# Kernel optimization log

Hardware: AMD Instinct MI355X
Metric: run time of the kernel (lower is better)

The kernel has to match this reference:

```python
import jax, jax.numpy as jnp
import numpy as np

SIZE = 128
N_ATOMS = 100000
N_BONDS = 400000
N_PAIRS = 400000
N_ANGLES = 800000
LN_EPS = 1e-5


def _layernorm(h, w, b):
    m = jnp.mean(h, axis=-1, keepdims=True)
    v = jnp.mean(jnp.square(h - m), axis=-1, keepdims=True)
    return (h - m) * jax.lax.rsqrt(v + LN_EPS) * w + b


def _forward(x, bond_x, sc_pair_x, angles,
             W_bm, W_sc, W1, b1, W2, b2,
             ln1_w, ln1_b, ln2_w, ln2_b,
             bond_idx, sc_idx, angles_idx):
    n_atoms = x.shape[0]
    n_bonds = bond_x.shape[0]

    # ---- sublayer 1: bond message passing ----
    h = _layernorm(x, ln1_w, ln1_b)                       # [n_atoms, d]
    # aggregate angle features onto bonds
    bond_ang = jax.ops.segment_sum(angles, angles_idx, num_segments=n_bonds)
    src, dst = bond_idx[:, 0], bond_idx[:, 1]
    msg = jax.nn.relu((h[src] + bond_x + bond_ang) @ W_bm)  # [n_bonds, d]
    agg = jax.ops.segment_sum(msg, dst, num_segments=n_atoms)
    x = x + (agg @ W1 + b1)                               # residual (dropout=0)

    # ---- sublayer 2: scalar-coupling pair message passing ----
    h2 = _layernorm(x, ln2_w, ln2_b)
    i, j = sc_idx[:, 0], sc_idx[:, 1]
    msg2 = jax.nn.relu((h2[i] + h2[j] + sc_pair_x) @ W_sc)  # [n_pairs, d]
    agg2 = jax.ops.segment_sum(msg2, i, num_segments=n_atoms)
    return x + (agg2 @ W2 + b2)


def setup_inputs() -> dict:
    key = jax.random.key(0)
    ks = jax.random.split(key, 16)
    s = 1.0 / np.sqrt(SIZE)
    inp = {
        "x": jax.random.normal(ks[0], (N_ATOMS, SIZE), jnp.float32),
        "bond_x": jax.random.normal(ks[1], (N_BONDS, SIZE), jnp.float32),
        "sc_pair_x": jax.random.normal(ks[2], (N_PAIRS, SIZE), jnp.float32),
        "angles": jax.random.normal(ks[3], (N_ANGLES, SIZE), jnp.float32),
        "W_bm": jax.random.normal(ks[4], (SIZE, SIZE), jnp.float32) * s,
        "W_sc": jax.random.normal(ks[5], (SIZE, SIZE), jnp.float32) * s,
        "W1": jax.random.normal(ks[6], (SIZE, SIZE), jnp.float32) * s,
        "b1": jnp.zeros((SIZE,), jnp.float32),
        "W2": jax.random.normal(ks[7], (SIZE, SIZE), jnp.float32) * s,
        "b2": jnp.zeros((SIZE,), jnp.float32),
        "ln1_w": jax.random.uniform(ks[8], (SIZE,), jnp.float32),
        "ln1_b": jnp.zeros((SIZE,), jnp.float32),
        "ln2_w": jax.random.uniform(ks[9], (SIZE,), jnp.float32),
        "ln2_b": jnp.zeros((SIZE,), jnp.float32),
        "mask": jnp.ones((N_ATOMS,), jnp.bool_),
        "bond_idx": jax.random.randint(ks[10], (N_BONDS, 2), 0, N_ATOMS),
        "sc_idx": jax.random.randint(ks[11], (N_PAIRS, 2), 0, N_ATOMS),
        "angles_idx": jax.random.randint(ks[12], (N_ANGLES,), 0, N_BONDS),
    }
    return inp


def reference(x, bond_x, sc_pair_x, angles, W_bm, W_sc, W1, b1, W2, b2,
              ln1_w, ln1_b, ln2_w, ln2_b, mask, bond_idx, sc_idx, angles_idx):
    # mask is in the torch forward signature but unused in its body
    return _forward(x, bond_x, sc_pair_x, angles, W_bm, W_sc, W1, b1, W2, b2,
                    ln1_w, ln1_b, ln2_w, ln2_b, bond_idx, sc_idx, angles_idx)
```

## Files before the change

kernel.cpp:

```cpp
#include <hip/hip_runtime.h>

#define SZ 128
#define NATOMS 100000
#define NBONDS 400000
#define NPAIRS 400000
#define NANG   800000

typedef float f32x4 __attribute__((ext_vector_type(4)));
typedef short s16x8 __attribute__((ext_vector_type(8)));

__device__ __forceinline__ unsigned short f2bf(float f) {
  union { float f; unsigned u; } v; v.f = f;
  unsigned r = v.u + 0x7FFFu + ((v.u >> 16) & 1u);
  return (unsigned short)(r >> 16);
}
__device__ __forceinline__ float bf2f(unsigned short h) {
  union { unsigned u; float f; } v; v.u = ((unsigned)h) << 16;
  return v.f;
}

#define AGG_OFF      0ull
#define AGG2_OFF     51200000ull
#define CNT_OFF      102400000ull
#define FILL_OFF     104000000ull
#define ZERO_BYTES   105600000ull
#define START_OFF    105600000ull
#define ALIST_OFF    107200000ull
#define BSUM_OFF     110400000ull
#define H_OFF        110404096ull
#define H2_OFF       136004096ull
#define WT_BM_OFF    161604096ull
#define WT_SC_OFF    (WT_BM_OFF + 32768ull)
#define WT1_OFF      (WT_SC_OFF + 32768ull)
#define WT2_OFF      (WT1_OFF + 32768ull)

#define SCAN_EPB 1024
#define NSCAN_BLOCKS ((NBONDS + SCAN_EPB - 1) / SCAN_EPB)

__global__ __launch_bounds__(256) void k_prep_w(const float* __restrict__ W,
                                                s16x8* __restrict__ Wt) {
  int cid = blockIdx.x * 256 + threadIdx.x;
  int nt8 = cid >> 8, kk = (cid >> 6) & 3, l = cid & 63;
  int col = nt8 * 16 + (l & 15);
  int k0  = kk * 32 + (l >> 4) * 8;
  s16x8 v;
#pragma unroll
  for (int i = 0; i < 8; ++i) v[i] = (short)f2bf(W[(k0 + i) * SZ + col]);
  Wt[cid] = v;
}

__global__ __launch_bounds__(256) void k_ln(const float* __restrict__ x,
                                            const float* __restrict__ g,
                                            const float* __restrict__ bvec,
                                            unsigned short* __restrict__ hout) {
  int row  = blockIdx.x * 4 + (threadIdx.x >> 6);
  int lane = threadIdx.x & 63;
  float2 v = *(const float2*)(x + (size_t)row * SZ + lane * 2);
  float s = v.x + v.y, sq = v.x * v.x + v.y * v.y;
#pragma unroll
  for (int off = 32; off; off >>= 1) { s += __shfl_xor(s, off); sq += __shfl_xor(sq, off); }
  float m = s * 0.0078125f;
  float var = sq * 0.0078125f - m * m;
  float rstd = rsqrtf(var + 1e-5f);
  float2 gv = *(const float2*)(g + lane * 2);
  float2 bv = *(const float2*)(bvec + lane * 2);
  float y0 = (v.x - m) * rstd * gv.x + bv.x;
  float y1 = (v.y - m) * rstd * gv.y + bv.y;
  unsigned pack = (unsigned)f2bf(y0) | ((unsigned)f2bf(y1) << 16);
  ((unsigned*)hout)[(size_t)row * 64 + lane] = pack;
}

__global__ __launch_bounds__(256) void k_hist(const int* __restrict__ aidx,
                                              int* __restrict__ cnt) {
  int id = blockIdx.x * 256 + threadIdx.x;
  if (id < NANG) atomicAdd(&cnt[aidx[id]], 1);
}

__global__ __launch_bounds__(256) void k_scan1(const int* __restrict__ cnt,
                                               int* __restrict__ start,
                                               int* __restrict__ bsum) {
  __shared__ int wsum[4];
  int tid = threadIdx.x, bid = blockIdx.x;
  int base = bid * SCAN_EPB + tid * 4;
  int4 c;
  if (base + 3 < NBONDS) {
    c = *(const int4*)(cnt + base);
  } else {
    c.x = (base + 0 < NBONDS) ? cnt[base + 0] : 0;
    c.y = (base + 1 < NBONDS) ? cnt[base + 1] : 0;
    c.z = (base + 2 < NBONDS) ? cnt[base + 2] : 0;
    c.w = (base + 3 < NBONDS) ? cnt[base + 3] : 0;
  }
  int tsum = c.x + c.y + c.z + c.w;
  int lane = tid & 63, wid = tid >> 6;
  int inc = tsum;
#pragma unroll
  for (int off = 1; off < 64; off <<= 1) {
    int o = __shfl_up(inc, off);
    if (lane >= off) inc += o;
  }
  if (lane == 63) wsum[wid] = inc;
  __syncthreads();
  int woff = 0;
#pragma unroll
  for (int wq = 0; wq < 4; ++wq) { if (wq < wid) woff += wsum[wq]; }
  int s0 = woff + inc - tsum;
  if (base + 0 < NBONDS) { start[base + 0] = s0; } s0 += c.x;
  if (base + 1 < NBONDS) { start[base + 1] = s0; } s0 += c.y;
  if (base + 2 < NBONDS) { start[base + 2] = s0; } s0 += c.z;
  if (base + 3 < NBONDS) { start[base + 3] = s0; }
  if (tid == 255) {
    int tot = 0;
#pragma unroll
    for (int wq = 0; wq < 4; ++wq) tot += wsum[wq];
    bsum[bid] = tot;
  }
}

__global__ __launch_bounds__(512) void k_scan2(int* __restrict__ bsum, int n) {
  __shared__ int tmp[2][512];
  int tid = threadIdx.x;
  tmp[0][tid] = (tid < n) ? bsum[tid] : 0;
  int pi = 0;
  for (int off = 1; off < 512; off <<= 1) {
    __syncthreads();
    int t = tmp[pi][tid];
    if (tid >= off) t += tmp[pi][tid - off];
    tmp[pi ^ 1][tid] = t;
    pi ^= 1;
  }
  __syncthreads();
  if (tid < n) bsum[tid] = (tid == 0) ? 0 : tmp[pi][tid - 1];
}

__global__ __launch_bounds__(256) void k_scan_add(int* __restrict__ start,
                                                  const int* __restrict__ bsum) {
  int id = blockIdx.x * 256 + threadIdx.x;
  if (id < NBONDS) start[id] += bsum[id / SCAN_EPB];
}

__global__ __launch_bounds__(256) void k_fill(const int* __restrict__ aidx,
                                              const int* __restrict__ start,
                                              int* __restrict__ fill,
                                              int* __restrict__ alist) {
  int id = blockIdx.x * 256 + threadIdx.x;
  if (id < NANG) {
    int b = aidx[id];
    int p = atomicAdd(&fill[b], 1);
    alist[start[b] + p] = id;
  }
}

__global__ __launch_bounds__(256) void k_msg1(const unsigned short* __restrict__ h,
                                              const float* __restrict__ bx,
                                              const float* __restrict__ angles,
                                              const int* __restrict__ start,
                                              const int* __restrict__ cnt,
                                              const int* __restrict__ alist,
                                              const int* __restrict__ bidx,
                                              const s16x8* __restrict__ Wt,
                                              float* __restrict__ agg) {
  __shared__ s16x8 Wl[2048];
  __shared__ s16x8 Tl[256];
  int tid = threadIdx.x;
  for (int i = tid; i < 2048; i += 256) Wl[i] = Wt[i];
  __syncthreads();
  int r = tid >> 4, kc = tid & 15;
  int w = tid >> 6, l = tid & 63;
  for (int tile = blockIdx.x; tile < NBONDS / 16; tile += gridDim.x) {
    int base = tile * 16;
    int b = base + r;
    int sidx = bidx[2 * b];
    uint4 hv = *(const uint4*)(h + (size_t)sidx * SZ + kc * 8);
    const unsigned short* hp = (const unsigned short*)&hv;
    float xb[8];
    *(float4*)&xb[0] = *(const float4*)(bx + (size_t)b * SZ + kc * 8);
    *(float4*)&xb[4] = *(const float4*)(bx + (size_t)b * SZ + kc * 8 + 4);
    float ab[8] = {0.f, 0.f, 0.f, 0.f, 0.f, 0.f, 0.f, 0.f};
    int s0 = start[b], nc = cnt[b];
    for (int t = 0; t < nc; ++t) {
      int ar = alist[s0 + t];
      const float* ap = angles + (size_t)ar * SZ + kc * 8;
      float4 u0 = *(const float4*)ap;
      float4 u1 = *(const float4*)(ap + 4);
      ab[0] += u0.x; ab[1] += u0.y; ab[2] += u0.z; ab[3] += u0.w;
      ab[4] += u1.x; ab[5] += u1.y; ab[6] += u1.z; ab[7] += u1.w;
    }
    s16x8 tv;
#pragma unroll
    for (int i = 0; i < 8; ++i) tv[i] = (short)f2bf(bf2f(hp[i]) + xb[i] + ab[i]);
    Tl[(kc >> 2) * 64 + (kc & 3) * 16 + r] = tv;
    __syncthreads();
    f32x4 acc0 = {0.f, 0.f, 0.f, 0.f}, acc1 = {0.f, 0.f, 0.f, 0.f};
#pragma unroll
    for (int kk = 0; kk < 4; ++kk) {
      s16x8 av = Tl[kk * 64 + l];
      acc0 = __builtin_amdgcn_mfma_f32_16x16x32_bf16(av, Wl[((w * 2 + 0) * 4 + kk) * 64 + l], acc0, 0, 0, 0);
      acc1 = __builtin_amdgcn_mfma_f32_16x16x32_bf16(av, Wl[((w * 2 + 1) * 4 + kk) * 64 + l], acc1, 0, 0, 0);
    }
    int colb = w * 32 + (l & 15);
    int rowb = (l >> 4) * 4;
#pragma unroll
    for (int p = 0; p < 4; ++p) {
      int bb = base + rowb + p;
      int d = bidx[2 * bb + 1];
      unsafeAtomicAdd(agg + (size_t)d * SZ + colb,      fmaxf(acc0[p], 0.f));
      unsafeAtomicAdd(agg + (size_t)d * SZ + colb + 16, fmaxf(acc1[p], 0.f));
    }
    __syncthreads();
  }
}

__global__ __launch_bounds__(256) void k_msg2(const unsigned short* __restrict__ h2,
                                              const float* __restrict__ scp,
                                              const int* __restrict__ sidx,
                                              const s16x8* __restrict__ Wt,
                                              float* __restrict__ agg2) {
  __shared__ s16x8 Wl[2048];
  __shared__ s16x8 Tl[256];
  int tid = threadIdx.x;
  for (int i = tid; i < 2048; i += 256) Wl[i] = Wt[i];
  __syncthreads();
  int r = tid >> 4, kc = tid & 15;
  int w = tid >> 6, l = tid & 63;
  for (int tile = blockIdx.x; tile < NPAIRS / 16; tile += gridDim.x) {
    int base = tile * 16;
    int b = base + r;
    int i0 = sidx[2 * b], j0 = sidx[2 * b + 1];
    uint4 hv1 = *(const uint4*)(h2 + (size_t)i0 * SZ + kc * 8);
    uint4 hv2 = *(const uint4*)(h2 + (size_t)j0 * SZ + kc * 8);
    const unsigned short* hp1 = (const unsigned short*)&hv1;
    const unsigned short* hp2 = (const unsigned short*)&hv2;
    float sb[8];
    *(float4*)&sb[0] = *(const float4*)(scp + (size_t)b * SZ + kc * 8);
    *(float4*)&sb[4] = *(const float4*)(scp + (size_t)b * SZ + kc * 8 + 4);
    s16x8 tv;
#pragma unroll
    for (int i = 0; i < 8; ++i) tv[i] = (short)f2bf(bf2f(hp1[i]) + bf2f(hp2[i]) + sb[i]);
    Tl[(kc >> 2) * 64 + (kc & 3) * 16 + r] = tv;
    __syncthreads();
    f32x4 acc0 = {0.f, 0.f, 0.f, 0.f}, acc1 = {0.f, 0.f, 0.f, 0.f};
#pragma unroll
    for (int kk = 0; kk < 4; ++kk) {
      s16x8 av = Tl[kk * 64 + l];
      acc0 = __builtin_amdgcn_mfma_f32_16x16x32_bf16(av, Wl[((w * 2 + 0) * 4 + kk) * 64 + l], acc0, 0, 0, 0);
      acc1 = __builtin_amdgcn_mfma_f32_16x16x32_bf16(av, Wl[((w * 2 + 1) * 4 + kk) * 64 + l], acc1, 0, 0, 0);
    }
    int colb = w * 32 + (l & 15);
    int rowb = (l >> 4) * 4;
#pragma unroll
    for (int p = 0; p < 4; ++p) {
      int bb = base + rowb + p;
      int d = sidx[2 * bb];
      unsafeAtomicAdd(agg2 + (size_t)d * SZ + colb,      fmaxf(acc0[p], 0.f));
      unsafeAtomicAdd(agg2 + (size_t)d * SZ + colb + 16, fmaxf(acc1[p], 0.f));
    }
    __syncthreads();
  }
}

__global__ __launch_bounds__(256) void k_update1(const float* __restrict__ agg,
                                                 const float* __restrict__ x,
                                                 const float* __restrict__ b1,
                                                 const float* __restrict__ lnw,
                                                 const float* __restrict__ lnb,
                                                 const s16x8* __restrict__ Wt,
                                                 float* __restrict__ out,
                                                 unsigned short* __restrict__ h2) {
  __shared__ s16x8 Wl[2048];
  __shared__ s16x8 Tl[256];
  __shared__ float Xl[16][128];
  int tid = threadIdx.x;
  for (int i = tid; i < 2048; i += 256) Wl[i] = Wt[i];
  __syncthreads();
  int r = tid >> 4, kc = tid & 15;
  int w = tid >> 6, l = tid & 63;
  int colb = w * 32 + (l & 15);
  int rowb = (l >> 4) * 4;
  float bb0 = b1[colb], bb1 = b1[colb + 16];
  float2 g2 = *(const float2*)(lnw + l * 2);
  float2 be2 = *(const float2*)(lnb + l * 2);
  for (int tile = blockIdx.x; tile < NATOMS / 16; tile += gridDim.x) {
    int base = tile * 16;
    int a = base + r;
    float qb[8];
    *(float4*)&qb[0] = *(const float4*)(agg + (size_t)a * SZ + kc * 8);
    *(float4*)&qb[4] = *(const float4*)(agg + (size_t)a * SZ + kc * 8 + 4);
    s16x8 tv;
#pragma unroll
    for (int i = 0; i < 8; ++i) tv[i] = (short)f2bf(qb[i]);
    Tl[(kc >> 2) * 64 + (kc & 3) * 16 + r] = tv;
    __syncthreads();
    f32x4 acc0 = {0.f, 0.f, 0.f, 0.f}, acc1 = {0.f, 0.f, 0.f, 0.f};
#pragma unroll
    for (int kk = 0; kk < 4; ++kk) {
      s16x8 av = Tl[kk * 64 + l];
      acc0 = __builtin_amdgcn_mfma_f32_16x16x32_bf16(av, Wl[((w * 2 + 0) * 4 + kk) * 64 + l], acc0, 0, 0, 0);
      acc1 = __builtin_amdgcn_mfma_f32_16x16x32_bf16(av, Wl[((w * 2 + 1) * 4 + kk) * 64 + l], acc1, 0, 0, 0);
    }
#pragma unroll
    for (int p = 0; p < 4; ++p) {
      int atom = base + rowb + p;
      float v0 = acc0[p] + bb0 + x[(size_t)atom * SZ + colb];
      float v1 = acc1[p] + bb1 + x[(size_t)atom * SZ + colb + 16];
      out[(size_t)atom * SZ + colb] = v0;
      out[(size_t)atom * SZ + colb + 16] = v1;
      Xl[rowb + p][colb] = v0;
      Xl[rowb + p][colb + 16] = v1;
    }
    __syncthreads();
#pragma unroll
    for (int rr = 0; rr < 4; ++rr) {
      int rw = w * 4 + rr;
      float2 v = *(const float2*)&Xl[rw][l * 2];
      float s = v.x + v.y, sq = v.x * v.x + v.y * v.y;
#pragma unroll
      for (int off = 32; off; off >>= 1) { s += __shfl_xor(s, off); sq += __shfl_xor(sq, off); }
      float m = s * 0.0078125f;
      float var = sq * 0.0078125f - m * m;
      float rstd = rsqrtf(var + 1e-5f);
      float y0 = (v.x - m) * rstd * g2.x + be2.x;
      float y1 = (v.y - m) * rstd * g2.y + be2.y;
      unsigned pack = (unsigned)f2bf(y0) | ((unsigned)f2bf(y1) << 16);
      ((unsigned*)h2)[(size_t)(base + rw) * 64 + l] = pack;
    }
    __syncthreads();
  }
}

__global__ __launch_bounds__(256) void k_update2(const float* __restrict__ agg2,
                                                 const float* __restrict__ b2,
                                                 const s16x8* __restrict__ Wt,
                                                 float* __restrict__ out) {
  __shared__ s16x8 Wl[2048];
  __shared__ s16x8 Tl[256];
  int tid = threadIdx.x;
  for (int i = tid; i < 2048; i += 256) Wl[i] = Wt[i];
  __syncthreads();
  int r = tid >> 4, kc = tid & 15;
  int w = tid >> 6, l = tid & 63;
  int colb = w * 32 + (l & 15);
  int rowb = (l >> 4) * 4;
  float bb0 = b2[colb], bb1 = b2[colb + 16];
  for (int tile = blockIdx.x; tile < NATOMS / 16; tile += gridDim.x) {
    int base = tile * 16;
    int a = base + r;
    float qb[8];
    *(float4*)&qb[0] = *(const float4*)(agg2 + (size_t)a * SZ + kc * 8);
    *(float4*)&qb[4] = *(const float4*)(agg2 + (size_t)a * SZ + kc * 8 + 4);
    s16x8 tv;
#pragma unroll
    for (int i = 0; i < 8; ++i) tv[i] = (short)f2bf(qb[i]);
    Tl[(kc >> 2) * 64 + (kc & 3) * 16 + r] = tv;
    __syncthreads();
    f32x4 acc0 = {0.f, 0.f, 0.f, 0.f}, acc1 = {0.f, 0.f, 0.f, 0.f};
#pragma unroll
    for (int kk = 0; kk < 4; ++kk) {
      s16x8 av = Tl[kk * 64 + l];
      acc0 = __builtin_amdgcn_mfma_f32_16x16x32_bf16(av, Wl[((w * 2 + 0) * 4 + kk) * 64 + l], acc0, 0, 0, 0);
      acc1 = __builtin_amdgcn_mfma_f32_16x16x32_bf16(av, Wl[((w * 2 + 1) * 4 + kk) * 64 + l], acc1, 0, 0, 0);
    }
#pragma unroll
    for (int p = 0; p < 4; ++p) {
      int atom = base + rowb + p;
      out[(size_t)atom * SZ + colb]      += acc0[p] + bb0;
      out[(size_t)atom * SZ + colb + 16] += acc1[p] + bb1;
    }
    __syncthreads();
  }
}

extern "C" void kernel_launch(void* const* d_in, const int* in_sizes, int n_in,
                              void* d_out, int out_size, void* d_ws, size_t ws_size,
                              hipStream_t stream) {
  (void)in_sizes; (void)n_in; (void)out_size; (void)ws_size;
  const float* x        = (const float*)d_in[0];
  const float* bond_x   = (const float*)d_in[1];
  const float* sc_pair  = (const float*)d_in[2];
  const float* angles   = (const float*)d_in[3];
  const float* W_bm     = (const float*)d_in[4];
  const float* W_sc     = (const float*)d_in[5];
  const float* W1       = (const float*)d_in[6];
  const float* b1       = (const float*)d_in[7];
  const float* W2       = (const float*)d_in[8];
  const float* b2       = (const float*)d_in[9];
  const float* ln1w     = (const float*)d_in[10];
  const float* ln1b     = (const float*)d_in[11];
  const float* ln2w     = (const float*)d_in[12];
  const float* ln2b     = (const float*)d_in[13];
  const int* bond_idx   = (const int*)d_in[15];
  const int* sc_idx     = (const int*)d_in[16];
  const int* ang_idx    = (const int*)d_in[17];
  float* out = (float*)d_out;
  char* ws = (char*)d_ws;

  float* agg      = (float*)(ws + AGG_OFF);
  float* agg2     = (float*)(ws + AGG2_OFF);
  int*   cnt      = (int*)(ws + CNT_OFF);
  int*   fill     = (int*)(ws + FILL_OFF);
  int*   start    = (int*)(ws + START_OFF);
  int*   alist    = (int*)(ws + ALIST_OFF);
  int*   bsum     = (int*)(ws + BSUM_OFF);
  unsigned short* hbuf  = (unsigned short*)(ws + H_OFF);
  unsigned short* h2buf = (unsigned short*)(ws + H2_OFF);
  s16x8* wt_bm = (s16x8*)(ws + WT_BM_OFF);
  s16x8* wt_sc = (s16x8*)(ws + WT_SC_OFF);
  s16x8* wt1   = (s16x8*)(ws + WT1_OFF);
  s16x8* wt2   = (s16x8*)(ws + WT2_OFF);

  hipMemsetAsync(ws, 0, ZERO_BYTES, stream);

  k_prep_w<<<8, 256, 0, stream>>>(W_bm, wt_bm);
  k_prep_w<<<8, 256, 0, stream>>>(W_sc, wt_sc);
  k_prep_w<<<8, 256, 0, stream>>>(W1, wt1);
  k_prep_w<<<8, 256, 0, stream>>>(W2, wt2);

  k_hist<<<(NANG + 255) / 256, 256, 0, stream>>>(ang_idx, cnt);
  k_scan1<<<NSCAN_BLOCKS, 256, 0, stream>>>(cnt, start, bsum);
  k_scan2<<<1, 512, 0, stream>>>(bsum, NSCAN_BLOCKS);
  k_scan_add<<<(NBONDS + 255) / 256, 256, 0, stream>>>(start, bsum);
  k_fill<<<(NANG + 255) / 256, 256, 0, stream>>>(ang_idx, start, fill, alist);

  k_ln<<<NATOMS / 4, 256, 0, stream>>>(x, ln1w, ln1b, hbuf);
  k_msg1<<<2048, 256, 0, stream>>>(hbuf, bond_x, angles, start, cnt, alist, bond_idx, wt_bm, agg);
  k_update1<<<1024, 256, 0, stream>>>(agg, x, b1, ln2w, ln2b, wt1, out, h2buf);
  k_msg2<<<2048, 256, 0, stream>>>(h2buf, sc_pair, sc_idx, wt_sc, agg2);
  k_update2<<<1024, 256, 0, stream>>>(agg2, b2, wt2, out);
}
```

Before: 655.5 us.

## Make message kernels wave-independent: one wave per 16-row tile, no LDS staging

k_msg1 and k_msg2 now give each wavefront its own 16-row tile and compute all 128 output columns (8 MFMA accumulators). The A-fragment is built directly in registers, so the LDS staging buffer and the per-tile __syncthreads are gone. k_msg1 also prefetches up to four angle indices and unconditionally loads their rows with zero weights to expose memory-level parallelism, then loops for any extra angles. The cost is higher register pressure (launch bounds 256,4) and redundant angle loads for bonds with fewer than four angles.

```diff
diff --git a/kernel.cpp b/kernel.cpp
--- a/kernel.cpp
+++ b/kernel.cpp
@@ -151,111 +151,134 @@
   }
 }
 
-__global__ __launch_bounds__(256) void k_msg1(const unsigned short* __restrict__ h,
-                                              const float* __restrict__ bx,
-                                              const float* __restrict__ angles,
-                                              const int* __restrict__ start,
-                                              const int* __restrict__ cnt,
-                                              const int* __restrict__ alist,
-                                              const int* __restrict__ bidx,
-                                              const s16x8* __restrict__ Wt,
-                                              float* __restrict__ agg) {
+__global__ __launch_bounds__(256, 4) void k_msg1(const unsigned short* __restrict__ h,
+                                                 const float* __restrict__ bx,
+                                                 const float* __restrict__ angles,
+                                                 const int* __restrict__ start,
+                                                 const int* __restrict__ cnt,
+                                                 const int* __restrict__ alist,
+                                                 const int* __restrict__ bidx,
+                                                 const s16x8* __restrict__ Wt,
+                                                 float* __restrict__ agg) {
   __shared__ s16x8 Wl[2048];
-  __shared__ s16x8 Tl[256];
   int tid = threadIdx.x;
   for (int i = tid; i < 2048; i += 256) Wl[i] = Wt[i];
   __syncthreads();
-  int r = tid >> 4, kc = tid & 15;
   int w = tid >> 6, l = tid & 63;
-  for (int tile = blockIdx.x; tile < NBONDS / 16; tile += gridDim.x) {
+  int grp = l >> 4;
+  int rl  = l & 15;
+  int gw = blockIdx.x * 4 + w;
+  int nw = gridDim.x * 4;
+  for (int tile = gw; tile < NBONDS / 16; tile += nw) {
     int base = tile * 16;
-    int b = base + r;
-    int sidx = bidx[2 * b];
-    uint4 hv = *(const uint4*)(h + (size_t)sidx * SZ + kc * 8);
-    const unsigned short* hp = (const unsigned short*)&hv;
-    float xb[8];
-    *(float4*)&xb[0] = *(const float4*)(bx + (size_t)b * SZ + kc * 8);
-    *(float4*)&xb[4] = *(const float4*)(bx + (size_t)b * SZ + kc * 8 + 4);
-    float ab[8] = {0.f, 0.f, 0.f, 0.f, 0.f, 0.f, 0.f, 0.f};
+    int b = base + rl;
+    int s = bidx[2 * b];
     int s0 = start[b], nc = cnt[b];
-    for (int t = 0; t < nc; ++t) {
-      int ar = alist[s0 + t];
-      const float* ap = angles + (size_t)ar * SZ + kc * 8;
-      float4 u0 = *(const float4*)ap;
-      float4 u1 = *(const float4*)(ap + 4);
-      ab[0] += u0.x; ab[1] += u0.y; ab[2] += u0.z; ab[3] += u0.w;
-      ab[4] += u1.x; ab[5] += u1.y; ab[6] += u1.z; ab[7] += u1.w;
-    }
-    s16x8 tv;
-#pragma unroll
-    for (int i = 0; i < 8; ++i) tv[i] = (short)f2bf(bf2f(hp[i]) + xb[i] + ab[i]);
-    Tl[(kc >> 2) * 64 + (kc & 3) * 16 + r] = tv;
-    __syncthreads();
-    f32x4 acc0 = {0.f, 0.f, 0.f, 0.f}, acc1 = {0.f, 0.f, 0.f, 0.f};
+    int aj[4];
+#pragma unroll
+    for (int t = 0; t < 4; ++t) {
+      int idx = s0 + (t < nc - 1 ? t : (nc > 0 ? nc - 1 : 0));
+      idx = idx < NANG - 1 ? idx : NANG - 1;
+      aj[t] = alist[idx];
+    }
+    f32x4 acc[8];
+#pragma unroll
+    for (int nb = 0; nb < 8; ++nb) acc[nb] = (f32x4){0.f, 0.f, 0.f, 0.f};
 #pragma unroll
     for (int kk = 0; kk < 4; ++kk) {
-      s16x8 av = Tl[kk * 64 + l];
-      acc0 = __builtin_amdgcn_mfma_f32_16x16x32_bf16(av, Wl[((w * 2 + 0) * 4 + kk) * 64 + l], acc0, 0, 0, 0);
-      acc1 = __builtin_amdgcn_mfma_f32_16x16x32_bf16(av, Wl[((w * 2 + 1) * 4 + kk) * 64 + l], acc1, 0, 0, 0);
-    }
-    int colb = w * 32 + (l & 15);
-    int rowb = (l >> 4) * 4;
+      const int co = kk * 32 + grp * 8;
+      uint4 hv = *(const uint4*)(h + (size_t)s * SZ + co);
+      float4 b0 = *(const float4*)(bx + (size_t)b * SZ + co);
+      float4 b1 = *(const float4*)(bx + (size_t)b * SZ + co + 4);
+      float a[8];
+      a[0] = b0.x; a[1] = b0.y; a[2] = b0.z; a[3] = b0.w;
+      a[4] = b1.x; a[5] = b1.y; a[6] = b1.z; a[7] = b1.w;
+#pragma unroll
+      for (int t = 0; t < 4; ++t) {
+        float wt = (t < nc) ? 1.f : 0.f;
+        const float* ap = angles + (size_t)aj[t] * SZ + co;
+        float4 u0 = *(const float4*)ap;
+        float4 u1 = *(const float4*)(ap + 4);
+        a[0] += wt * u0.x; a[1] += wt * u0.y; a[2] += wt * u0.z; a[3] += wt * u0.w;
+        a[4] += wt * u1.x; a[5] += wt * u1.y; a[6] += wt * u1.z; a[7] += wt * u1.w;
+      }
+      for (int t = 4; t < nc; ++t) {
+        int ar = alist[s0 + t];
+        const float* ap = angles + (size_t)ar * SZ + co;
+        float4 u0 = *(const float4*)ap;
+        float4 u1 = *(const float4*)(ap + 4);
+        a[0] += u0.x; a[1] += u0.y; a[2] += u0.z; a[3] += u0.w;
+        a[4] += u1.x; a[5] += u1.y; a[6] += u1.z; a[7] += u1.w;
+      }
+      const unsigned short* hp = (const unsigned short*)&hv;
+      s16x8 af;
+#pragma unroll
+      for (int i = 0; i < 8; ++i) af[i] = (short)f2bf(bf2f(hp[i]) + a[i]);
+#pragma unroll
+      for (int nb = 0; nb < 8; ++nb)
+        acc[nb] = __builtin_amdgcn_mfma_f32_16x16x32_bf16(af, Wl[(nb * 4 + kk) * 64 + l], acc[nb], 0, 0, 0);
+    }
 #pragma unroll
     for (int p = 0; p < 4; ++p) {
-      int bb = base + rowb + p;
-      int d = bidx[2 * bb + 1];
-      unsafeAtomicAdd(agg + (size_t)d * SZ + colb,      fmaxf(acc0[p], 0.f));
-      unsafeAtomicAdd(agg + (size_t)d * SZ + colb + 16, fmaxf(acc1[p], 0.f));
-    }
-    __syncthreads();
-  }
-}
-
-__global__ __launch_bounds__(256) void k_msg2(const unsigned short* __restrict__ h2,
-                                              const float* __restrict__ scp,
-                                              const int* __restrict__ sidx,
-                                              const s16x8* __restrict__ Wt,
-                                              float* __restrict__ agg2) {
+      int row = base + grp * 4 + p;
+      int d = bidx[2 * row + 1];
+      float* pb = agg + (size_t)d * SZ + rl;
+#pragma unroll
+      for (int nb = 0; nb < 8; ++nb)
+        unsafeAtomicAdd(pb + nb * 16, fmaxf(acc[nb][p], 0.f));
+    }
+  }
+}
+
+__global__ __launch_bounds__(256, 4) void k_msg2(const unsigned short* __restrict__ h2,
+                                                 const float* __restrict__ scp,
+                                                 const int* __restrict__ sidx,
+                                                 const s16x8* __restrict__ Wt,
+                                                 float* __restrict__ agg2) {
   __shared__ s16x8 Wl[2048];
-  __shared__ s16x8 Tl[256];
   int tid = threadIdx.x;
   for (int i = tid; i < 2048; i += 256) Wl[i] = Wt[i];
   __syncthreads();
-  int r = tid >> 4, kc = tid & 15;
   int w = tid >> 6, l = tid & 63;
-  for (int tile = blockIdx.x; tile < NPAIRS / 16; tile += gridDim.x) {
+  int grp = l >> 4;
+  int rl  = l & 15;
+  int gw = blockIdx.x * 4 + w;
+  int nw = gridDim.x * 4;
+  for (int tile = gw; tile < NPAIRS / 16; tile += nw) {
     int base = tile * 16;
-    int b = base + r;
+    int b = base + rl;
     int i0 = sidx[2 * b], j0 = sidx[2 * b + 1];
-    uint4 hv1 = *(const uint4*)(h2 + (size_t)i0 * SZ + kc * 8);
-    uint4 hv2 = *(const uint4*)(h2 + (size_t)j0 * SZ + kc * 8);
-    const unsigned short* hp1 = (const unsigned short*)&hv1;
-    const unsigned short* hp2 = (const unsigned short*)&hv2;
-    float sb[8];
-    *(float4*)&sb[0] = *(const float4*)(scp + (size_t)b * SZ + kc * 8);
-    *(float4*)&sb[4] = *(const float4*)(scp + (size_t)b * SZ + kc * 8 + 4);
-    s16x8 tv;
-#pragma unroll
-    for (int i = 0; i < 8; ++i) tv[i] = (short)f2bf(bf2f(hp1[i]) + bf2f(hp2[i]) + sb[i]);
-    Tl[(kc >> 2) * 64 + (kc & 3) * 16 + r] = tv;
-    __syncthreads();
-    f32x4 acc0 = {0.f, 0.f, 0.f, 0.f}, acc1 = {0.f, 0.f, 0.f, 0.f};
+    f32x4 acc[8];
+#pragma unroll
+    for (int nb = 0; nb < 8; ++nb) acc[nb] = (f32x4){0.f, 0.f, 0.f, 0.f};
 #pragma unroll
     for (int kk = 0; kk < 4; ++kk) {
-      s16x8 av = Tl[kk * 64 + l];
-      acc0 = __builtin_amdgcn_mfma_f32_16x16x32_bf16(av, Wl[((w * 2 + 0) * 4 + kk) * 64 + l], acc0, 0, 0, 0);
-      acc1 = __builtin_amdgcn_mfma_f32_16x16x32_bf16(av, Wl[((w * 2 + 1) * 4 + kk) * 64 + l], acc1, 0, 0, 0);
-    }
-    int colb = w * 32 + (l & 15);
-    int rowb = (l >> 4) * 4;
+      const int co = kk * 32 + grp * 8;
+      uint4 hv1 = *(const uint4*)(h2 + (size_t)i0 * SZ + co);
+      uint4 hv2 = *(const uint4*)(h2 + (size_t)j0 * SZ + co);
+      float4 s0v = *(const float4*)(scp + (size_t)b * SZ + co);
+      float4 s1v = *(const float4*)(scp + (size_t)b * SZ + co + 4);
+      const unsigned short* p1 = (const unsigned short*)&hv1;
+      const unsigned short* p2 = (const unsigned short*)&hv2;
+      float a[8];
+      a[0] = s0v.x; a[1] = s0v.y; a[2] = s0v.z; a[3] = s0v.w;
+      a[4] = s1v.x; a[5] = s1v.y; a[6] = s1v.z; a[7] = s1v.w;
+      s16x8 af;
+#pragma unroll
+      for (int i = 0; i < 8; ++i) af[i] = (short)f2bf(bf2f(p1[i]) + bf2f(p2[i]) + a[i]);
+#pragma unroll
+      for (int nb = 0; nb < 8; ++nb)
+        acc[nb] = __builtin_amdgcn_mfma_f32_16x16x32_bf16(af, Wl[(nb * 4 + kk) * 64 + l], acc[nb], 0, 0, 0);
+    }
 #pragma unroll
     for (int p = 0; p < 4; ++p) {
-      int bb = base + rowb + p;
-      int d = sidx[2 * bb];
-      unsafeAtomicAdd(agg2 + (size_t)d * SZ + colb,      fmaxf(acc0[p], 0.f));
-      unsafeAtomicAdd(agg2 + (size_t)d * SZ + colb + 16, fmaxf(acc1[p], 0.f));
-    }
-    __syncthreads();
+      int row = base + grp * 4 + p;
+      int d = sidx[2 * row];
+      float* pb = agg2 + (size_t)d * SZ + rl;
+#pragma unroll
+      for (int nb = 0; nb < 8; ++nb)
+        unsafeAtomicAdd(pb + nb * 16, fmaxf(acc[nb][p], 0.f));
+    }
   }
 }
 
```

Result: slower. 822.8 us (+25.5%).
